# Kernel optimization log

Hardware: AMD Instinct MI355X
Metric: run time of the kernel (lower is better)

Reference implementation:

```python
import jax, jax.numpy as jnp
import numpy as np

DIM = 1536
HEADS = 12
HD = DIM // HEADS           # 128
C = HD // 2                 # 64 rotary pairs per head
B = 1
F_, H_, W_ = 16, 16, 16
S = F_ * H_ * W_            # 4096
MAXPOS = 1024
EPS = 1e-6
SPLITS = (C - 2 * (C // 3), C // 3, C // 3)  # (22, 21, 21)


def setup_inputs() -> dict:
    key = jax.random.key(0)
    ks = jax.random.split(key, 8)
    std = 0.02
    x = jax.random.normal(ks[0], (B, S, DIM), jnp.float32)
    seq_lens = jnp.full((B,), S, dtype=jnp.int32)
    grid_sizes = jnp.tile(jnp.array([[F_, H_, W_]], jnp.int32), (B, 1))
    # rotary angle table: per split, theta_j = pos / 10000^(j/size)
    angs = []
    pos = jnp.arange(MAXPOS, dtype=jnp.float32)
    for sz in SPLITS:
        inv = 1.0 / (10000.0 ** (jnp.arange(sz, dtype=jnp.float32) / sz))
        angs.append(jnp.outer(pos, inv))
    freqs = jnp.concatenate(angs, axis=1)  # [MAXPOS, C]
    return {
        "x": x,
        "seq_lens": seq_lens,
        "grid_sizes": grid_sizes,
        "freqs": freqs,
        "wq": jax.random.normal(ks[1], (DIM, DIM), jnp.float32) * std,
        "bq": jnp.zeros((DIM,), jnp.float32),
        "wk": jax.random.normal(ks[2], (DIM, DIM), jnp.float32) * std,
        "bk": jnp.zeros((DIM,), jnp.float32),
        "wv": jax.random.normal(ks[3], (DIM, DIM), jnp.float32) * std,
        "bv": jnp.zeros((DIM,), jnp.float32),
        "wo": jax.random.normal(ks[4], (DIM, DIM), jnp.float32) * std,
        "bo": jnp.zeros((DIM,), jnp.float32),
        "gq": jnp.ones((DIM,), jnp.float32),
        "gk": jnp.ones((DIM,), jnp.float32),
    }


def _rms_norm(x, g):
    # x * rsqrt(mean(x^2) + eps) * g  (WanRMSNorm)
    var = jnp.mean(jnp.square(x), axis=-1, keepdims=True)
    return x * jax.lax.rsqrt(var + EPS) * g


def _rope(x, freqs, f, h, w):
    # x: [b, s, n, hd]; freqs: [MAXPOS, C] angles; grid (f,h,w), s = f*h*w
    fa = freqs[:f, : SPLITS[0]]
    ha = freqs[:h, SPLITS[0] : SPLITS[0] + SPLITS[1]]
    wa = freqs[:w, SPLITS[0] + SPLITS[1] :]
    ang = jnp.concatenate(
        [
            jnp.broadcast_to(fa[:, None, None, :], (f, h, w, SPLITS[0])),
            jnp.broadcast_to(ha[None, :, None, :], (f, h, w, SPLITS[1])),
            jnp.broadcast_to(wa[None, None, :, :], (f, h, w, SPLITS[2])),
        ],
        axis=-1,
    ).reshape(f * h * w, 1, C)  # [s, 1, C] broadcasts over heads
    cos, sin = jnp.cos(ang), jnp.sin(ang)
    xr = x[..., 0::2]  # real parts of complex pairs
    xi = x[..., 1::2]  # imag parts
    out_r = xr * cos - xi * sin
    out_i = xr * sin + xi * cos
    return jnp.stack([out_r, out_i], axis=-1).reshape(x.shape)


def reference(x, seq_lens, grid_sizes, freqs, wq, bq, wk, bk, wv, bv, wo, bo, gq, gk):
    b, s = x.shape[:2]
    q = _rms_norm(x @ wq.T + bq, gq).reshape(b, s, HEADS, HD)
    k = _rms_norm(x @ wk.T + bk, gk).reshape(b, s, HEADS, HD)
    v = (x @ wv.T + bv).reshape(b, s, HEADS, HD)
    # all samples share the same grid (static for jit)
    q = _rope(q, freqs, F_, H_, W_)
    k = _rope(k, freqs, F_, H_, W_)
    scale = 1.0 / np.sqrt(HD)
    scores = jnp.einsum("bqnd,bknd->bnqk", q, k) * scale  # [b, n, s, s]
    k_pos = jnp.arange(s)
    mask = k_pos[None, None, None, :] < seq_lens[:, None, None, None]
    scores = scores + jnp.where(mask, 0.0, -1e9)
    attn = jax.nn.softmax(scores, axis=-1)
    out = jnp.einsum("bnqk,bknd->bqnd", attn, v).reshape(b, s, DIM)
    return out @ wo.T + bo
```

## Files before the change

### kernel.cpp

```cpp
#include <hip/hip_runtime.h>
#include <hip/hip_bf16.h>

#define DIM   1536
#define HEADS 12
#define HD    128
#define SEQ   4096
#define QSCALE 0.08838834764831845f
#define LOG2E 1.44269504088896f

typedef __attribute__((ext_vector_type(8))) short short8;
typedef __attribute__((ext_vector_type(4))) float f32x4;
typedef __attribute__((ext_vector_type(16))) float f32x16;

__device__ __forceinline__ unsigned short f2bf(float f) {
    __hip_bfloat16 h = __float2bfloat16(f);
    return *reinterpret_cast<unsigned short*>(&h);
}
__device__ __forceinline__ float bf2f(unsigned short u) {
    return __uint_as_float(((unsigned int)u) << 16);
}
__device__ __forceinline__ void async_cp16(void* lds, const void* g) {
    __builtin_amdgcn_global_load_lds(
        (const __attribute__((address_space(1))) unsigned int*)g,
        (__attribute__((address_space(3))) unsigned int*)lds, 16, 0, 0);
}

__global__ __launch_bounds__(256) void convert_bf16(
    const float* __restrict__ src, __hip_bfloat16* __restrict__ dst, int n8)
{
    const int i = blockIdx.x * 256 + threadIdx.x;
    if (i >= n8) return;
    const float4 a = *reinterpret_cast<const float4*>(src + (size_t)i * 8);
    const float4 b = *reinterpret_cast<const float4*>(src + (size_t)i * 8 + 4);
    uint4 o;
    o.x = (unsigned int)f2bf(a.x) | ((unsigned int)f2bf(a.y) << 16);
    o.y = (unsigned int)f2bf(a.z) | ((unsigned int)f2bf(a.w) << 16);
    o.z = (unsigned int)f2bf(b.x) | ((unsigned int)f2bf(b.y) << 16);
    o.w = (unsigned int)f2bf(b.z) | ((unsigned int)f2bf(b.w) << 16);
    *reinterpret_cast<uint4*>(dst + (size_t)i * 8) = o;
}

__global__ __launch_bounds__(256) void gemm_qkv(
    const __hip_bfloat16* __restrict__ xb,
    const __hip_bfloat16* __restrict__ wqb, const float* __restrict__ bq,
    const __hip_bfloat16* __restrict__ wkb, const float* __restrict__ bk,
    const __hip_bfloat16* __restrict__ wvb, const float* __restrict__ bv,
    __hip_bfloat16* __restrict__ yq, __hip_bfloat16* __restrict__ yk,
    __hip_bfloat16* __restrict__ vrow)
{
    __shared__ __align__(16) short As[128][32];
    __shared__ __align__(16) short Bs[128][32];
    const int z  = blockIdx.z;
    const __hip_bfloat16* W = (z == 0) ? wqb : (z == 1) ? wkb : wvb;
    const float* bias = (z == 0) ? bq : (z == 1) ? bk : bv;
    __hip_bfloat16* outp = (z == 0) ? yq : (z == 1) ? yk : vrow;
    const int bm0 = blockIdx.x * 128;
    const int bn0 = blockIdx.y * 128;
    const int tid  = threadIdx.x;
    const int lane = tid & 63;
    const int wid  = tid >> 6;
    const int wm = (wid >> 1) * 64;
    const int wn = (wid & 1)  * 64;
    const int fr = lane & 15;
    const int fc = (lane >> 4) * 8;
    const int srow = tid >> 2;
    const int scol = (tid & 3) * 8;

    f32x4 acc[4][4] = {};

    for (int kt = 0; kt < DIM; kt += 32) {
        #pragma unroll
        for (int i = 0; i < 2; i++) {
            async_cp16(&As[i * 64 + ((tid >> 6) << 4)][0],
                       xb + (size_t)(bm0 + i * 64 + srow) * DIM + kt + scol);
            async_cp16(&Bs[i * 64 + ((tid >> 6) << 4)][0],
                       W + (size_t)(bn0 + i * 64 + srow) * DIM + kt + scol);
        }
        __syncthreads();
        short8 af[4], bf8[4];
        #pragma unroll
        for (int m = 0; m < 4; m++) af[m]  = *reinterpret_cast<const short8*>(&As[wm + m * 16 + fr][fc]);
        #pragma unroll
        for (int n = 0; n < 4; n++) bf8[n] = *reinterpret_cast<const short8*>(&Bs[wn + n * 16 + fr][fc]);
        #pragma unroll
        for (int m = 0; m < 4; m++)
            #pragma unroll
            for (int n = 0; n < 4; n++)
                acc[m][n] = __builtin_amdgcn_mfma_f32_16x16x32_bf16(af[m], bf8[n], acc[m][n], 0, 0, 0);
        __syncthreads();
    }

    const int crow0 = bm0 + wm + (lane >> 4) * 4;
    const int ccol0 = bn0 + wn + fr;
    #pragma unroll
    for (int n = 0; n < 4; n++) {
        const int col = ccol0 + n * 16;
        const float bb = bias[col];
        #pragma unroll
        for (int m = 0; m < 4; m++)
            #pragma unroll
            for (int r = 0; r < 4; r++)
                outp[(size_t)(crow0 + m * 16 + r) * DIM + col] =
                    __float2bfloat16(acc[m][n][r] + bb);
    }
}

__global__ __launch_bounds__(256) void rmsnorm_rope(
    __hip_bfloat16* __restrict__ yq, __hip_bfloat16* __restrict__ yk,
    const float* __restrict__ gq, const float* __restrict__ gk,
    const float* __restrict__ freqs)
{
    const int s = blockIdx.x;
    const int z = blockIdx.y;
    __hip_bfloat16* y = z ? yk : yq;
    const float* g = z ? gk : gq;
    const int t = threadIdx.x;

    float xr[3], xi[3];
    float ss = 0.f;
    #pragma unroll
    for (int i = 0; i < 3; i++) {
        const int p = t + i * 256;
        const unsigned int uu = *reinterpret_cast<const unsigned int*>(&y[(size_t)s * DIM + 2 * p]);
        xr[i] = bf2f((unsigned short)(uu & 0xffffu));
        xi[i] = bf2f((unsigned short)(uu >> 16));
        ss += xr[i] * xr[i] + xi[i] * xi[i];
    }
    #pragma unroll
    for (int m = 1; m < 64; m <<= 1) ss += __shfl_xor(ss, m, 64);
    __shared__ float red[4];
    if ((t & 63) == 0) red[t >> 6] = ss;
    __syncthreads();
    const float sum = red[0] + red[1] + red[2] + red[3];
    const float rs = rsqrtf(sum * (1.0f / DIM) + 1e-6f);
    const int f = s >> 8, hh = (s >> 4) & 15, ww = s & 15;
    const float osc = z ? 1.0f : QSCALE;
    #pragma unroll
    for (int i = 0; i < 3; i++) {
        const int p = t + i * 256;
        const int cc = p & 63;
        const int pos = (cc < 22) ? f : (cc < 43) ? hh : ww;
        const float ang = freqs[pos * 64 + cc];
        float sn, cs;
        sincosf(ang, &sn, &cs);
        const float a = xr[i] * rs * g[2 * p];
        const float b = xi[i] * rs * g[2 * p + 1];
        const unsigned int pk = (unsigned int)f2bf((a * cs - b * sn) * osc)
                              | ((unsigned int)f2bf((a * sn + b * cs) * osc) << 16);
        *reinterpret_cast<unsigned int*>(&y[(size_t)s * DIM + 2 * p]) = pk;
    }
}

__global__ __launch_bounds__(256) void transpose_v(
    const __hip_bfloat16* __restrict__ vrow,
    __hip_bfloat16* __restrict__ vT)
{
    __shared__ __align__(16) short tile[64][72];
    const int s0 = blockIdx.x * 64;
    const int c0 = blockIdx.y * 64;
    const int t = threadIdx.x;
    #pragma unroll
    for (int i = 0; i < 2; i++) {
        const int ch = t + i * 256;
        const int r = ch >> 3, cc = (ch & 7) * 8;
        *reinterpret_cast<int4*>(&tile[r][cc]) =
            *reinterpret_cast<const int4*>(&vrow[(size_t)(s0 + r) * DIM + c0 + cc]);
    }
    __syncthreads();
    #pragma unroll
    for (int i = 0; i < 2; i++) {
        const int ch = t + i * 256;
        const int c = ch & 63, sc = (ch >> 6) * 8;
        unsigned int w0 = (unsigned short)tile[sc + 0][c] | ((unsigned int)(unsigned short)tile[sc + 1][c] << 16);
        unsigned int w1 = (unsigned short)tile[sc + 2][c] | ((unsigned int)(unsigned short)tile[sc + 3][c] << 16);
        unsigned int w2 = (unsigned short)tile[sc + 4][c] | ((unsigned int)(unsigned short)tile[sc + 5][c] << 16);
        unsigned int w3 = (unsigned short)tile[sc + 6][c] | ((unsigned int)(unsigned short)tile[sc + 7][c] << 16);
        int4 val;
        val.x = (int)w0; val.y = (int)w1; val.z = (int)w2; val.w = (int)w3;
        *reinterpret_cast<int4*>(&vT[(size_t)(c0 + c) * SEQ + s0 + sc]) = val;
    }
}

__global__ __launch_bounds__(256, 3) void flash_attn(
    const __hip_bfloat16* __restrict__ qb,
    const __hip_bfloat16* __restrict__ kb,
    const __hip_bfloat16* __restrict__ vT,
    const int* __restrict__ seq_lens,
    __hip_bfloat16* __restrict__ attno)
{
    __shared__ __align__(16) short Ks[2][64][128];
    __shared__ __align__(16) short Vs[128][64];
    const int qt = blockIdx.x;
    const int h  = blockIdx.y;
    const int tid = threadIdx.x;
    const int lane = tid & 63;
    const int w = tid >> 6;
    const int q5 = lane & 31;
    const int hi = lane >> 5;
    const int seqlen = seq_lens[0];
    const int swz = (lane & 7) << 4;

    short8 qf[8];
    const int qrow = qt * 128 + w * 32 + q5;
    #pragma unroll
    for (int s = 0; s < 8; s++)
        qf[s] = *reinterpret_cast<const short8*>(&qb[(size_t)qrow * DIM + h * HD + s * 16 + hi * 8]);

    f32x16 oacc[4] = {};
    float m = -1e30f, l = 0.f;

    const int kROW = w * 4 + (lane >> 4);
    const int kCOL = ((lane & 15) ^ (kROW & 7)) * 8;
    const int vROW = w * 8 + (lane >> 3);
    const int vCOL = (((lane & 7) ^ (vROW & 7))) * 8;

    #pragma unroll
    for (int i = 0; i < 4; i++)
        async_cp16(&Ks[0][i * 16 + w * 4][0],
                   kb + (size_t)(i * 16 + kROW) * DIM + h * HD + kCOL);

    for (int t = 0; t < SEQ / 64; t++) {
        const int kbase = t * 64;
        __syncthreads();

        #pragma unroll
        for (int i = 0; i < 4; i++)
            async_cp16(&Vs[i * 32 + vROW][0],
                       vT + ((size_t)h * HD + i * 32 + vROW) * SEQ + kbase + vCOL);
        if (t + 1 < SEQ / 64) {
            const int nb = kbase + 64;
            #pragma unroll
            for (int i = 0; i < 4; i++)
                async_cp16(&Ks[(t + 1) & 1][i * 16 + w * 4][0],
                           kb + (size_t)(nb + i * 16 + kROW) * DIM + h * HD + kCOL);
        }

        const char* Kp = (const char*)&Ks[t & 1][0][0];

        f32x16 sacc[2] = {};
        __builtin_amdgcn_s_setprio(1);
        #pragma unroll
        for (int s = 0; s < 8; s++) {
            #pragma unroll
            for (int kbk = 0; kbk < 2; kbk++) {
                short8 kf = *reinterpret_cast<const short8*>(
                    Kp + (kbk * 32 + q5) * 256 + ((s * 32 + hi * 16) ^ swz));
                sacc[kbk] = __builtin_amdgcn_mfma_f32_32x32x16_bf16(kf, qf[s], sacc[kbk], 0, 0, 0);
            }
        }
        __builtin_amdgcn_s_setprio(0);

        float tmax = -1e30f;
        if (kbase + 64 <= seqlen) {
            #pragma unroll
            for (int kbk = 0; kbk < 2; kbk++)
                #pragma unroll
                for (int r = 0; r < 16; r++) tmax = fmaxf(tmax, sacc[kbk][r]);
        } else {
            #pragma unroll
            for (int kbk = 0; kbk < 2; kbk++) {
                #pragma unroll
                for (int r = 0; r < 16; r++) {
                    const int key = kbase + kbk * 32 + (r & 3) + 8 * (r >> 2) + 4 * hi;
                    const float sv = (key < seqlen) ? sacc[kbk][r] : -1e30f;
                    sacc[kbk][r] = sv;
                    tmax = fmaxf(tmax, sv);
                }
            }
        }
        tmax = fmaxf(tmax, __shfl_xor(tmax, 32, 64));

        if (!__all(tmax <= m + 8.0f)) {
            const float mn = fmaxf(m, tmax);
            const float alpha = exp2f((m - mn) * LOG2E);
            m = mn;
            l *= alpha;
            #pragma unroll
            for (int cb = 0; cb < 4; cb++)
                #pragma unroll
                for (int r = 0; r < 16; r++) oacc[cb][r] *= alpha;
        }

        float ps = 0.f;
        #pragma unroll
        for (int kbk = 0; kbk < 2; kbk++) {
            #pragma unroll
            for (int r = 0; r < 16; r++) {
                const float p = exp2f((sacc[kbk][r] - m) * LOG2E);
                sacc[kbk][r] = p;
                ps += p;
            }
        }
        ps += __shfl_xor(ps, 32, 64);
        l += ps;

        unsigned int W[2][4][2];
        #pragma unroll
        for (int kbk = 0; kbk < 2; kbk++)
            #pragma unroll
            for (int tq = 0; tq < 4; tq++) {
                W[kbk][tq][0] = (unsigned int)f2bf(sacc[kbk][4 * tq + 0])
                              | ((unsigned int)f2bf(sacc[kbk][4 * tq + 1]) << 16);
                W[kbk][tq][1] = (unsigned int)f2bf(sacc[kbk][4 * tq + 2])
                              | ((unsigned int)f2bf(sacc[kbk][4 * tq + 3]) << 16);
            }

        __syncthreads();

        const char* Vp = (const char*)&Vs[0][0];
        #pragma unroll
        for (int ks = 0; ks < 4; ks++) {
            const int kbk = ks >> 1;
            const int te = (ks & 1) * 2, to = te + 1;
            const int a0 = (int)W[kbk][te][0], a1 = (int)W[kbk][te][1];
            const int b0 = (int)W[kbk][to][0], b1 = (int)W[kbk][to][1];
            const int xa0 = __shfl_xor(a0, 32, 64);
            const int xa1 = __shfl_xor(a1, 32, 64);
            const int xb0 = __shfl_xor(b0, 32, 64);
            const int xb1 = __shfl_xor(b1, 32, 64);
            int4 pwv;
            pwv.x = hi ? xb0 : a0;
            pwv.y = hi ? xb1 : a1;
            pwv.z = hi ? b0  : xa0;
            pwv.w = hi ? b1  : xa1;
            const short8 pf = __builtin_bit_cast(short8, pwv);
            __builtin_amdgcn_s_setprio(1);
            #pragma unroll
            for (int cb = 0; cb < 4; cb++) {
                short8 vf = *reinterpret_cast<const short8*>(
                    Vp + (cb * 32 + q5) * 128 + ((ks * 32 + hi * 16) ^ swz));
                oacc[cb] = __builtin_amdgcn_mfma_f32_32x32x16_bf16(vf, pf, oacc[cb], 0, 0, 0);
            }
            __builtin_amdgcn_s_setprio(0);
        }
    }

    const float inv_l = 1.f / l;
    const size_t obase = (size_t)qrow * DIM + h * HD;
    #pragma unroll
    for (int cb = 0; cb < 4; cb++) {
        #pragma unroll
        for (int tq = 0; tq < 4; tq++) {
            uint2 pko;
            pko.x = (unsigned int)f2bf(oacc[cb][4 * tq + 0] * inv_l)
                  | ((unsigned int)f2bf(oacc[cb][4 * tq + 1] * inv_l) << 16);
            pko.y = (unsigned int)f2bf(oacc[cb][4 * tq + 2] * inv_l)
                  | ((unsigned int)f2bf(oacc[cb][4 * tq + 3] * inv_l) << 16);
            *reinterpret_cast<uint2*>(&attno[obase + cb * 32 + 8 * tq + 4 * hi]) = pko;
        }
    }
}

__global__ __launch_bounds__(256) void gemm_out(
    const __hip_bfloat16* __restrict__ A,
    const __hip_bfloat16* __restrict__ W,
    const float* __restrict__ bias,
    float* __restrict__ outp)
{
    __shared__ __align__(16) short As[128][32];
    __shared__ __align__(16) short Bs[128][32];
    const int bm0 = blockIdx.x * 128;
    const int bn0 = blockIdx.y * 128;
    const int tid = threadIdx.x;
    const int lane = tid & 63;
    const int wid = tid >> 6;
    const int wm = (wid >> 1) * 64;
    const int wn = (wid & 1) * 64;
    const int fr = lane & 15;
    const int fc = (lane >> 4) * 8;
    const int srow = tid >> 2;
    const int scol = (tid & 3) * 8;

    f32x4 acc[4][4] = {};

    for (int kt = 0; kt < DIM; kt += 32) {
        #pragma unroll
        for (int i = 0; i < 2; i++) {
            async_cp16(&As[i * 64 + ((tid >> 6) << 4)][0],
                       A + (size_t)(bm0 + i * 64 + srow) * DIM + kt + scol);
            async_cp16(&Bs[i * 64 + ((tid >> 6) << 4)][0],
                       W + (size_t)(bn0 + i * 64 + srow) * DIM + kt + scol);
        }
        __syncthreads();
        short8 af[4], bf8[4];
        #pragma unroll
        for (int m = 0; m < 4; m++) af[m]  = *reinterpret_cast<const short8*>(&As[wm + m * 16 + fr][fc]);
        #pragma unroll
        for (int n = 0; n < 4; n++) bf8[n] = *reinterpret_cast<const short8*>(&Bs[wn + n * 16 + fr][fc]);
        #pragma unroll
        for (int m = 0; m < 4; m++)
            #pragma unroll
            for (int n = 0; n < 4; n++)
                acc[m][n] = __builtin_amdgcn_mfma_f32_16x16x32_bf16(af[m], bf8[n], acc[m][n], 0, 0, 0);
        __syncthreads();
    }

    const int crow0 = bm0 + wm + (lane >> 4) * 4;
    const int ccol0 = bn0 + wn + fr;
    #pragma unroll
    for (int n = 0; n < 4; n++) {
        const int col = ccol0 + n * 16;
        const float bb = bias[col];
        #pragma unroll
        for (int m = 0; m < 4; m++)
            #pragma unroll
            for (int r = 0; r < 4; r++)
                outp[(size_t)(crow0 + m * 16 + r) * DIM + col] = acc[m][n][r] + bb;
    }
}

extern "C" void kernel_launch(void* const* d_in, const int* in_sizes, int n_in,
                              void* d_out, int out_size, void* d_ws, size_t ws_size,
                              hipStream_t stream)
{
    const float* x        = (const float*)d_in[0];
    const int*   seq_lens = (const int*)d_in[1];
    const float* freqs    = (const float*)d_in[3];
    const float* wq = (const float*)d_in[4];
    const float* bq = (const float*)d_in[5];
    const float* wk = (const float*)d_in[6];
    const float* bk = (const float*)d_in[7];
    const float* wv = (const float*)d_in[8];
    const float* bv = (const float*)d_in[9];
    const float* wo = (const float*)d_in[10];
    const float* bo = (const float*)d_in[11];
    const float* gq = (const float*)d_in[12];
    const float* gk = (const float*)d_in[13];
    float* out = (float*)d_out;

    char* ws = (char*)d_ws;
    __hip_bfloat16* yq    = (__hip_bfloat16*)(ws);
    __hip_bfloat16* yk    = (__hip_bfloat16*)(ws + 12582912);
    __hip_bfloat16* vrow  = (__hip_bfloat16*)(ws + 25165824);
    __hip_bfloat16* vT    = (__hip_bfloat16*)(ws + 37748736);
    __hip_bfloat16* attno = (__hip_bfloat16*)(ws + 25165824);
    __hip_bfloat16* xb    = (__hip_bfloat16*)(ws + 37748736);
    __hip_bfloat16* wob   = (__hip_bfloat16*)(ws);
    __hip_bfloat16* wqb   = (__hip_bfloat16*)d_out;
    __hip_bfloat16* wkb   = wqb + 2359296;
    __hip_bfloat16* wvb   = wkb + 2359296;

    dim3 blk(256);
    convert_bf16<<<dim3(3072), blk, 0, stream>>>(x,  xb,  786432);
    convert_bf16<<<dim3(1152), blk, 0, stream>>>(wq, wqb, 294912);
    convert_bf16<<<dim3(1152), blk, 0, stream>>>(wk, wkb, 294912);
    convert_bf16<<<dim3(1152), blk, 0, stream>>>(wv, wvb, 294912);
    gemm_qkv    <<<dim3(32, 12, 3), blk, 0, stream>>>(xb, wqb, bq, wkb, bk, wvb, bv, yq, yk, vrow);
    rmsnorm_rope<<<dim3(4096, 2),   blk, 0, stream>>>(yq, yk, gq, gk, freqs);
    transpose_v <<<dim3(64, 24),    blk, 0, stream>>>(vrow, vT);
    flash_attn  <<<dim3(32, 12),    blk, 0, stream>>>(yq, yk, vT, seq_lens, attno);
    convert_bf16<<<dim3(1152), blk, 0, stream>>>(wo, wob, 294912);
    gemm_out    <<<dim3(32, 12),    blk, 0, stream>>>(attno, wob, bo, out);
}
```

Measured before the change: 365.4 us.

## Software-pipeline flash attention to overlap QK, softmax and PV across tiles

Restructures the flash-attention main loop into a staggered pipeline. Each iteration computes QK^T for tile t+1, PV for tile t-1 and softmax for tile t, so matrix-core work can overlap the exp and max arithmetic. V staging becomes triple-buffered in LDS and the two score accumulators alternate via a manual 2x unrolled loop, with a prologue and epilogue for the first and last tiles. This adds register and LDS pressure, so the occupancy hint drops from 3 to 2 blocks per CU, which may weaken latency hiding.

```diff
diff --git a/kernel.cpp b/kernel.cpp
--- a/kernel.cpp
+++ b/kernel.cpp
@@ -181,7 +181,7 @@
     }
 }
 
-__global__ __launch_bounds__(256, 3) void flash_attn(
+__global__ __launch_bounds__(256, 2) void flash_attn(
     const __hip_bfloat16* __restrict__ qb,
     const __hip_bfloat16* __restrict__ kb,
     const __hip_bfloat16* __restrict__ vT,
@@ -189,7 +189,7 @@
     __hip_bfloat16* __restrict__ attno)
 {
     __shared__ __align__(16) short Ks[2][64][128];
-    __shared__ __align__(16) short Vs[128][64];
+    __shared__ __align__(16) short Vs[3][128][64];
     const int qt = blockIdx.x;
     const int h  = blockIdx.y;
     const int tid = threadIdx.x;
@@ -199,6 +199,7 @@
     const int hi = lane >> 5;
     const int seqlen = seq_lens[0];
     const int swz = (lane & 7) << 4;
+    const int NT = SEQ / 64;
 
     short8 qf[8];
     const int qrow = qt * 128 + w * 32 + q5;
@@ -208,36 +209,30 @@
 
     f32x16 oacc[4] = {};
     float m = -1e30f, l = 0.f;
+    unsigned int Wp[2][4][2];
+    f32x16 saccA[2], saccB[2];
 
     const int kROW = w * 4 + (lane >> 4);
     const int kCOL = ((lane & 15) ^ (kROW & 7)) * 8;
     const int vROW = w * 8 + (lane >> 3);
     const int vCOL = (((lane & 7) ^ (vROW & 7))) * 8;
 
-    #pragma unroll
-    for (int i = 0; i < 4; i++)
-        async_cp16(&Ks[0][i * 16 + w * 4][0],
-                   kb + (size_t)(i * 16 + kROW) * DIM + h * HD + kCOL);
-
-    for (int t = 0; t < SEQ / 64; t++) {
-        const int kbase = t * 64;
-        __syncthreads();
-
+    auto stageK = [&](int tile, int slot) {
         #pragma unroll
         for (int i = 0; i < 4; i++)
-            async_cp16(&Vs[i * 32 + vROW][0],
-                       vT + ((size_t)h * HD + i * 32 + vROW) * SEQ + kbase + vCOL);
-        if (t + 1 < SEQ / 64) {
-            const int nb = kbase + 64;
-            #pragma unroll
-            for (int i = 0; i < 4; i++)
-                async_cp16(&Ks[(t + 1) & 1][i * 16 + w * 4][0],
-                           kb + (size_t)(nb + i * 16 + kROW) * DIM + h * HD + kCOL);
-        }
-
-        const char* Kp = (const char*)&Ks[t & 1][0][0];
-
-        f32x16 sacc[2] = {};
+            async_cp16(&Ks[slot][i * 16 + w * 4][0],
+                       kb + (size_t)(tile * 64 + i * 16 + kROW) * DIM + h * HD + kCOL);
+    };
+    auto stageV = [&](int tile, int slot) {
+        #pragma unroll
+        for (int i = 0; i < 4; i++)
+            async_cp16(&Vs[slot][i * 32 + vROW][0],
+                       vT + ((size_t)h * HD + i * 32 + vROW) * SEQ + tile * 64 + vCOL);
+    };
+    auto qk = [&](int slot, f32x16* S) {
+        const char* Kp = (const char*)&Ks[slot][0][0];
+        S[0] = (f32x16){};
+        S[1] = (f32x16){};
         __builtin_amdgcn_s_setprio(1);
         #pragma unroll
         for (int s = 0; s < 8; s++) {
@@ -245,75 +240,19 @@
             for (int kbk = 0; kbk < 2; kbk++) {
                 short8 kf = *reinterpret_cast<const short8*>(
                     Kp + (kbk * 32 + q5) * 256 + ((s * 32 + hi * 16) ^ swz));
-                sacc[kbk] = __builtin_amdgcn_mfma_f32_32x32x16_bf16(kf, qf[s], sacc[kbk], 0, 0, 0);
+                S[kbk] = __builtin_amdgcn_mfma_f32_32x32x16_bf16(kf, qf[s], S[kbk], 0, 0, 0);
             }
         }
         __builtin_amdgcn_s_setprio(0);
-
-        float tmax = -1e30f;
-        if (kbase + 64 <= seqlen) {
-            #pragma unroll
-            for (int kbk = 0; kbk < 2; kbk++)
-                #pragma unroll
-                for (int r = 0; r < 16; r++) tmax = fmaxf(tmax, sacc[kbk][r]);
-        } else {
-            #pragma unroll
-            for (int kbk = 0; kbk < 2; kbk++) {
-                #pragma unroll
-                for (int r = 0; r < 16; r++) {
-                    const int key = kbase + kbk * 32 + (r & 3) + 8 * (r >> 2) + 4 * hi;
-                    const float sv = (key < seqlen) ? sacc[kbk][r] : -1e30f;
-                    sacc[kbk][r] = sv;
-                    tmax = fmaxf(tmax, sv);
-                }
-            }
-        }
-        tmax = fmaxf(tmax, __shfl_xor(tmax, 32, 64));
-
-        if (!__all(tmax <= m + 8.0f)) {
-            const float mn = fmaxf(m, tmax);
-            const float alpha = exp2f((m - mn) * LOG2E);
-            m = mn;
-            l *= alpha;
-            #pragma unroll
-            for (int cb = 0; cb < 4; cb++)
-                #pragma unroll
-                for (int r = 0; r < 16; r++) oacc[cb][r] *= alpha;
-        }
-
-        float ps = 0.f;
-        #pragma unroll
-        for (int kbk = 0; kbk < 2; kbk++) {
-            #pragma unroll
-            for (int r = 0; r < 16; r++) {
-                const float p = exp2f((sacc[kbk][r] - m) * LOG2E);
-                sacc[kbk][r] = p;
-                ps += p;
-            }
-        }
-        ps += __shfl_xor(ps, 32, 64);
-        l += ps;
-
-        unsigned int W[2][4][2];
-        #pragma unroll
-        for (int kbk = 0; kbk < 2; kbk++)
-            #pragma unroll
-            for (int tq = 0; tq < 4; tq++) {
-                W[kbk][tq][0] = (unsigned int)f2bf(sacc[kbk][4 * tq + 0])
-                              | ((unsigned int)f2bf(sacc[kbk][4 * tq + 1]) << 16);
-                W[kbk][tq][1] = (unsigned int)f2bf(sacc[kbk][4 * tq + 2])
-                              | ((unsigned int)f2bf(sacc[kbk][4 * tq + 3]) << 16);
-            }
-
-        __syncthreads();
-
-        const char* Vp = (const char*)&Vs[0][0];
+    };
+    auto pv = [&](int slot) {
+        const char* Vp = (const char*)&Vs[slot][0][0];
         #pragma unroll
         for (int ks = 0; ks < 4; ks++) {
             const int kbk = ks >> 1;
             const int te = (ks & 1) * 2, to = te + 1;
-            const int a0 = (int)W[kbk][te][0], a1 = (int)W[kbk][te][1];
-            const int b0 = (int)W[kbk][to][0], b1 = (int)W[kbk][to][1];
+            const int a0 = (int)Wp[kbk][te][0], a1 = (int)Wp[kbk][te][1];
+            const int b0 = (int)Wp[kbk][to][0], b1 = (int)Wp[kbk][to][1];
             const int xa0 = __shfl_xor(a0, 32, 64);
             const int xa1 = __shfl_xor(a1, 32, 64);
             const int xb0 = __shfl_xor(b0, 32, 64);
@@ -333,7 +272,85 @@
             }
             __builtin_amdgcn_s_setprio(0);
         }
-    }
+    };
+    auto softmax_step = [&](int tt, f32x16* S) {
+        const int kbase = tt * 64;
+        float tmax = -1e30f;
+        if (kbase + 64 <= seqlen) {
+            #pragma unroll
+            for (int kbk = 0; kbk < 2; kbk++)
+                #pragma unroll
+                for (int r = 0; r < 16; r++) tmax = fmaxf(tmax, S[kbk][r]);
+        } else {
+            #pragma unroll
+            for (int kbk = 0; kbk < 2; kbk++)
+                #pragma unroll
+                for (int r = 0; r < 16; r++) {
+                    const int key = kbase + kbk * 32 + (r & 3) + 8 * (r >> 2) + 4 * hi;
+                    const float sv = (key < seqlen) ? S[kbk][r] : -1e30f;
+                    S[kbk][r] = sv;
+                    tmax = fmaxf(tmax, sv);
+                }
+        }
+        tmax = fmaxf(tmax, __shfl_xor(tmax, 32, 64));
+        if (!__all(tmax <= m + 8.0f)) {
+            const float mn = fmaxf(m, tmax);
+            const float alpha = exp2f((m - mn) * LOG2E);
+            m = mn;
+            l *= alpha;
+            #pragma unroll
+            for (int cb = 0; cb < 4; cb++)
+                #pragma unroll
+                for (int r = 0; r < 16; r++) oacc[cb][r] *= alpha;
+        }
+        float ps = 0.f;
+        #pragma unroll
+        for (int kbk = 0; kbk < 2; kbk++)
+            #pragma unroll
+            for (int r = 0; r < 16; r++) {
+                const float p = exp2f((S[kbk][r] - m) * LOG2E);
+                S[kbk][r] = p;
+                ps += p;
+            }
+        ps += __shfl_xor(ps, 32, 64);
+        l += ps;
+        #pragma unroll
+        for (int kbk = 0; kbk < 2; kbk++)
+            #pragma unroll
+            for (int tq = 0; tq < 4; tq++) {
+                Wp[kbk][tq][0] = (unsigned int)f2bf(S[kbk][4 * tq + 0])
+                               | ((unsigned int)f2bf(S[kbk][4 * tq + 1]) << 16);
+                Wp[kbk][tq][1] = (unsigned int)f2bf(S[kbk][4 * tq + 2])
+                               | ((unsigned int)f2bf(S[kbk][4 * tq + 3]) << 16);
+            }
+    };
+    auto iter_body = [&](int t, f32x16* Scur, f32x16* Snxt) {
+        __syncthreads();
+        stageV(t + 1, (t + 1) % 3);
+        if (t + 2 < NT) stageK(t + 2, t & 1);
+        qk((t + 1) & 1, Snxt);
+        pv((t - 1) % 3);
+        softmax_step(t, Scur);
+    };
+
+    stageK(0, 0); stageV(0, 0);
+    __syncthreads();
+    stageK(1, 1); stageV(1, 1);
+    qk(0, saccA);
+    __syncthreads();
+    stageK(2, 0);
+    qk(1, saccB);
+    softmax_step(0, saccA);
+
+    for (int t = 1; t + 1 <= NT - 2; t += 2) {
+        iter_body(t,     saccB, saccA);
+        iter_body(t + 1, saccA, saccB);
+    }
+
+    __syncthreads();
+    pv((NT - 2) % 3);
+    softmax_step(NT - 1, saccB);
+    pv((NT - 1) % 3);
 
     const float inv_l = 1.f / l;
     const size_t obase = (size_t)qrow * DIM + h * HD;
```

New measurement: 328.9 us. 1.11x faster.
